# Performance work log

Measured on AMD Instinct MI355X. Metric: run time of the kernel, lower is better.

The kernel has to match this reference:

```python
import math
import jax, jax.numpy as jnp
import numpy as np

VMIN, VMAX, NUM_BINS = 0.0, 1.0, 64
BIN_WIDTH = (VMAX - VMIN) / NUM_BINS
SIGMA = BIN_WIDTH * (1.0 / (2.0 * math.sqrt(2.0 * math.log(2.0))))
EPS = 1e-10


def setup_inputs() -> dict:
    key = jax.random.key(0)
    kx, ky = jax.random.split(key)
    shape = (2, 1, 96, 96, 96)
    x = jax.random.uniform(kx, shape, dtype=jnp.float32)
    y = jax.random.uniform(ky, shape, dtype=jnp.float32)
    return {"x": x, "y": y}


def _gauss_win(v, bins):
    # v: (N, P), bins: (B,) -> (N, B, P)
    d = v[:, None, :] - bins[None, :, None]
    # NOTE: faithful to source: exp(.)/sqrt(2*pi) * sigma (multiplies by sigma)
    return jnp.exp(-(d * d) / (2.0 * SIGMA * SIGMA)) / math.sqrt(2.0 * math.pi) * SIGMA


def reference(x, y):
    N = x.shape[0]
    xf = x.reshape(N, -1)  # (N, P); dim=1 channel folded into P
    yf = y.reshape(N, -1)
    bins = jnp.linspace(VMIN, VMAX, NUM_BINS, dtype=x.dtype)
    win_x = _gauss_win(xf, bins)  # (N, B, P)
    win_y = _gauss_win(yf, bins)  # (N, B, P)
    hist_joint = jnp.einsum('nbp,ncp->nbc', win_x, win_y)  # (N, B, B)
    hist_norm = hist_joint.sum(axis=(1, 2)) + EPS
    p_joint = hist_joint / hist_norm[:, None, None]
    p_x = p_joint.sum(axis=2)
    p_y = p_joint.sum(axis=1)
    ent_x = -jnp.sum(p_x * jnp.log(p_x + EPS), axis=1)
    ent_y = -jnp.sum(p_y * jnp.log(p_y + EPS), axis=1)
    ent_joint = -jnp.sum(p_joint * jnp.log(p_joint + EPS), axis=(1, 2))
    # normalised=True branch
    return -jnp.mean((ent_x + ent_y) / ent_joint)
```

## Files before the change

kernel.cpp:

```cpp
#include <hip/hip_runtime.h>
#include <math.h>


#define NBINS 64
#define BK 240
#define LDA 248
#define NKB 15

typedef _Float16 half8    __attribute__((ext_vector_type(8)));
typedef float    floatx16 __attribute__((ext_vector_type(16)));

static constexpr double kSigmaD = 0.015625 / 2.3548200450309493;
static constexpr double kAcD    = (1.0 / (63.0 * 63.0)) / (2.0 * kSigmaD * kSigmaD);
static constexpr float  kAc     = (float)kAcD;
static constexpr float  kEps    = 1e-10f;

__device__ __forceinline__ void make_weights(float vx, float vy, bool valid,
                                             int& cx, int& cy,
                                             float* wx, float* wy) {
    cx = 2; cy = 2;
#pragma unroll
    for (int k = 0; k < 5; ++k) { wx[k] = 0.0f; wy[k] = 0.0f; }
    if (valid) {
        cx = min(max((int)(vx + 0.5f), 2), 61);
        cy = min(max((int)(vy + 0.5f), 2), 61);
        const float dx = vx - (float)cx;
        const float dy = vy - (float)cy;
#pragma unroll
        for (int k = 0; k < 5; ++k) {
            const float ddx = dx - (float)(k - 2);
            const float ddy = dy - (float)(k - 2);
            wx[k] = __expf(-kAc * ddx * ddx);
            wy[k] = __expf(-kAc * ddy * ddy);
        }
    }
}

__global__ __launch_bounds__(256) void hist_gemm_kernel(
        const float* __restrict__ x, const float* __restrict__ y,
        float* __restrict__ hist, int P, int elemsPerBlock) {
    __shared__ __align__(16) _Float16 tiles[2 * NBINS * LDA];
    _Float16* Ax = tiles;
    _Float16* By = tiles + NBINS * LDA;

    const int t    = threadIdx.x;
    const int lane = t & 63;
    const int wave = t >> 6;
    const int m    = lane & 31;
    const int kq   = 8 * (lane >> 5);
    const int n    = blockIdx.y;

    {
        float* z4 = (float*)tiles;
        const int ndw = 2 * NBINS * LDA / 2;
        for (int i = t; i < ndw; i += 256) z4[i] = 0.0f;
    }

    floatx16 acc[2][2];
#pragma unroll
    for (int bi = 0; bi < 2; ++bi)
#pragma unroll
        for (int bj = 0; bj < 2; ++bj) acc[bi][bj] = (floatx16){};

    const float* __restrict__ xp = x + (size_t)n * P;
    const float* __restrict__ yp = y + (size_t)n * P;
    const int base    = blockIdx.x * elemsPerBlock;
    const int nElems  = elemsPerBlock;
    const int nChunks = (nElems + BK - 1) / BK;

    int cx, cy; float wx[5], wy[5];
    {
        const bool valid = (t < BK) && (t < nElems);
        float vx = 0.0f, vy = 0.0f;
        if (valid) { vx = xp[base + t] * 63.0f; vy = yp[base + t] * 63.0f; }
        make_weights(vx, vy, valid, cx, cy, wx, wy);
    }
    int pcx = 2, pcy = 2;
    __syncthreads();

    for (int c = 0; c < nChunks; ++c) {
        if (t < BK) {
#pragma unroll
            for (int k = 0; k < 5; ++k) {
                Ax[(pcx - 2 + k) * LDA + t] = (_Float16)0.0f;
                By[(pcy - 2 + k) * LDA + t] = (_Float16)0.0f;
            }
#pragma unroll
            for (int k = 0; k < 5; ++k) {
                Ax[(cx - 2 + k) * LDA + t] = (_Float16)wx[k];
                By[(cy - 2 + k) * LDA + t] = (_Float16)wy[k];
            }
        }
        pcx = cx; pcy = cy;
        __syncthreads();

        float vx = 0.0f, vy = 0.0f; bool valid = false;
        if (c + 1 < nChunks) {
            const int off = (c + 1) * BK + t;
            valid = (t < BK) && (off < nElems);
            if (valid) { vx = xp[base + off] * 63.0f; vy = yp[base + off] * 63.0f; }
        }

#pragma unroll
        for (int s = 0; s < 4; ++s) {
            const int kb = wave + 4 * s;
            if (kb >= NKB) break;
            const int ko = kb * 16 + kq;
            const half8 a0 = *(const half8*)&Ax[m * LDA + ko];
            const half8 a1 = *(const half8*)&Ax[(32 + m) * LDA + ko];
            const half8 b0 = *(const half8*)&By[m * LDA + ko];
            const half8 b1 = *(const half8*)&By[(32 + m) * LDA + ko];
            acc[0][0] = __builtin_amdgcn_mfma_f32_32x32x16_f16(a0, b0, acc[0][0], 0, 0, 0);
            acc[0][1] = __builtin_amdgcn_mfma_f32_32x32x16_f16(a0, b1, acc[0][1], 0, 0, 0);
            acc[1][0] = __builtin_amdgcn_mfma_f32_32x32x16_f16(a1, b0, acc[1][0], 0, 0, 0);
            acc[1][1] = __builtin_amdgcn_mfma_f32_32x32x16_f16(a1, b1, acc[1][1], 0, 0, 0);
        }

        make_weights(vx, vy, valid, cx, cy, wx, wy);
        __syncthreads();
    }

    float* cred = (float*)tiles;
    const int rbase = 4 * (lane >> 5);

    if (wave >= 2) {
        const int off = (wave - 2) * 4096;
#pragma unroll
        for (int bi = 0; bi < 2; ++bi)
#pragma unroll
            for (int bj = 0; bj < 2; ++bj)
#pragma unroll
                for (int r = 0; r < 16; ++r) {
                    const int row = bi * 32 + (r & 3) + 8 * (r >> 2) + rbase;
                    const int col = bj * 32 + m;
                    cred[off + row * NBINS + col] = acc[bi][bj][r];
                }
    }
    __syncthreads();
    if (wave < 2) {
        const int off = wave * 4096;
#pragma unroll
        for (int bi = 0; bi < 2; ++bi)
#pragma unroll
            for (int bj = 0; bj < 2; ++bj)
#pragma unroll
                for (int r = 0; r < 16; ++r) {
                    const int row = bi * 32 + (r & 3) + 8 * (r >> 2) + rbase;
                    const int col = bj * 32 + m;
                    const int idx = off + row * NBINS + col;
                    cred[idx] = acc[bi][bj][r] + cred[idx];
                }
    }
    __syncthreads();
    float* __restrict__ gh = hist + (size_t)n * NBINS * NBINS;
    for (int i = t; i < NBINS * NBINS; i += 256)
        atomicAdd(&gh[i], cred[i] + cred[4096 + i]);
}

__device__ __forceinline__ float block_sum_bcast(float v, float* sm) {
#pragma unroll
    for (int off = 32; off > 0; off >>= 1) v += __shfl_down(v, off, 64);
    __syncthreads();
    const int lane = threadIdx.x & 63;
    const int wid  = threadIdx.x >> 6;
    if (lane == 0) sm[wid] = v;
    __syncthreads();
    return sm[0] + sm[1] + sm[2] + sm[3];
}

__global__ __launch_bounds__(256) void finalize_kernel(
        const float* __restrict__ hist, float* __restrict__ out) {
    __shared__ float sm[4];
    __shared__ float sx[NBINS];
    __shared__ float sy[NBINS];

    const int n = blockIdx.x;
    const float* __restrict__ h = hist + (size_t)n * NBINS * NBINS;

    float s = 0.0f;
    for (int i = threadIdx.x; i < NBINS * NBINS; i += 256) s += h[i];
    const float S = block_sum_bcast(s, sm) + kEps;
    const float invS = 1.0f / S;

    float ej = 0.0f;
    for (int i = threadIdx.x; i < NBINS * NBINS; i += 256) {
        const float p = h[i] * invS;
        ej += p * __logf(p + kEps);
    }

    if (threadIdx.x < NBINS) {
        float px = 0.0f;
        const float* rp = &h[threadIdx.x * NBINS];
        for (int c = 0; c < NBINS; c++) px += rp[c];
        px *= invS;
        sx[threadIdx.x] = px * __logf(px + kEps);
    } else if (threadIdx.x < 2 * NBINS) {
        const int c = threadIdx.x - NBINS;
        float py = 0.0f;
        for (int b = 0; b < NBINS; b++) py += h[b * NBINS + c];
        py *= invS;
        sy[c] = py * __logf(py + kEps);
    }

    const float EJ = block_sum_bcast(ej, sm);
    const float mx = (threadIdx.x < NBINS) ? sx[threadIdx.x] : 0.0f;
    const float my = (threadIdx.x < NBINS) ? sy[threadIdx.x] : 0.0f;
    const float EX = block_sum_bcast(mx, sm);
    const float EY = block_sum_bcast(my, sm);

    if (threadIdx.x == 0) atomicAdd(out, -0.5f * ((EX + EY) / EJ));
}

extern "C" void kernel_launch(void* const* d_in, const int* in_sizes, int n_in,
                              void* d_out, int out_size, void* d_ws, size_t ws_size,
                              hipStream_t stream) {
    const float* x = (const float*)d_in[0];
    const float* y = (const float*)d_in[1];
    float* hist = (float*)d_ws;
    float* out  = (float*)d_out;

    const int N = 2;
    const int P = in_sizes[0] / N;
    const int blocksPerN = 256;
    const int elemsPerBlock = P / blocksPerN;

    hipMemsetAsync(hist, 0, (size_t)N * NBINS * NBINS * sizeof(float), stream);
    hipMemsetAsync(out, 0, sizeof(float), stream);

    dim3 grid(blocksPerN, N);
    hist_gemm_kernel<<<grid, 256, 0, stream>>>(x, y, hist, P, elemsPerBlock);

    finalize_kernel<<<2, 256, 0, stream>>>(hist, out);
}
```

Measured before the change: 107.8 us.

## Split output quadrants across waves, shrink K chunk, and raise block count

Each wave now owns one 32x32 quadrant of the 64x64 joint histogram and runs the full K range of each chunk, replacing the earlier scheme where waves split K and summed four accumulators. The chunk size drops to 112 elements, blocksPerN grows to 576, and launch bounds request more resident blocks. The intermediate shared-memory reduction goes away and each wave atomically adds its accumulators straight to global memory. The aim is more parallelism and less per-block reduction work, at the cost of more global atomics and more blocks contending on the same histogram entries.

```diff
diff --git a/kernel.cpp b/kernel.cpp
--- a/kernel.cpp
+++ b/kernel.cpp
@@ -3,9 +3,9 @@
 
 
 #define NBINS 64
-#define BK 240
-#define LDA 248
-#define NKB 15
+#define BK 112
+#define LDA 120
+#define NKB 7
 
 typedef _Float16 half8    __attribute__((ext_vector_type(8)));
 typedef float    floatx16 __attribute__((ext_vector_type(16)));
@@ -36,7 +36,7 @@
     }
 }
 
-__global__ __launch_bounds__(256) void hist_gemm_kernel(
+__global__ __launch_bounds__(256, 4) void hist_gemm_kernel(
         const float* __restrict__ x, const float* __restrict__ y,
         float* __restrict__ hist, int P, int elemsPerBlock) {
     __shared__ __align__(16) _Float16 tiles[2 * NBINS * LDA];
@@ -48,6 +48,8 @@
     const int wave = t >> 6;
     const int m    = lane & 31;
     const int kq   = 8 * (lane >> 5);
+    const int qi   = wave >> 1;
+    const int qj   = wave & 1;
     const int n    = blockIdx.y;
 
     {
@@ -56,11 +58,7 @@
         for (int i = t; i < ndw; i += 256) z4[i] = 0.0f;
     }
 
-    floatx16 acc[2][2];
-#pragma unroll
-    for (int bi = 0; bi < 2; ++bi)
-#pragma unroll
-        for (int bj = 0; bj < 2; ++bj) acc[bi][bj] = (floatx16){};
+    floatx16 acc = {};
 
     const float* __restrict__ xp = x + (size_t)n * P;
     const float* __restrict__ yp = y + (size_t)n * P;
@@ -101,60 +99,27 @@
             if (valid) { vx = xp[base + off] * 63.0f; vy = yp[base + off] * 63.0f; }
         }
 
+        const int rA = qi * 32 + m;
+        const int rB = qj * 32 + m;
 #pragma unroll
-        for (int s = 0; s < 4; ++s) {
-            const int kb = wave + 4 * s;
-            if (kb >= NKB) break;
-            const int ko = kb * 16 + kq;
-            const half8 a0 = *(const half8*)&Ax[m * LDA + ko];
-            const half8 a1 = *(const half8*)&Ax[(32 + m) * LDA + ko];
-            const half8 b0 = *(const half8*)&By[m * LDA + ko];
-            const half8 b1 = *(const half8*)&By[(32 + m) * LDA + ko];
-            acc[0][0] = __builtin_amdgcn_mfma_f32_32x32x16_f16(a0, b0, acc[0][0], 0, 0, 0);
-            acc[0][1] = __builtin_amdgcn_mfma_f32_32x32x16_f16(a0, b1, acc[0][1], 0, 0, 0);
-            acc[1][0] = __builtin_amdgcn_mfma_f32_32x32x16_f16(a1, b0, acc[1][0], 0, 0, 0);
-            acc[1][1] = __builtin_amdgcn_mfma_f32_32x32x16_f16(a1, b1, acc[1][1], 0, 0, 0);
+        for (int kb = 0; kb < NKB; ++kb) {
+            const half8 a = *(const half8*)&Ax[rA * LDA + kb * 16 + kq];
+            const half8 b = *(const half8*)&By[rB * LDA + kb * 16 + kq];
+            acc = __builtin_amdgcn_mfma_f32_32x32x16_f16(a, b, acc, 0, 0, 0);
         }
 
         make_weights(vx, vy, valid, cx, cy, wx, wy);
         __syncthreads();
     }
 
-    float* cred = (float*)tiles;
+    float* __restrict__ gh = hist + (size_t)n * NBINS * NBINS;
     const int rbase = 4 * (lane >> 5);
-
-    if (wave >= 2) {
-        const int off = (wave - 2) * 4096;
 #pragma unroll
-        for (int bi = 0; bi < 2; ++bi)
-#pragma unroll
-            for (int bj = 0; bj < 2; ++bj)
-#pragma unroll
-                for (int r = 0; r < 16; ++r) {
-                    const int row = bi * 32 + (r & 3) + 8 * (r >> 2) + rbase;
-                    const int col = bj * 32 + m;
-                    cred[off + row * NBINS + col] = acc[bi][bj][r];
-                }
+    for (int r = 0; r < 16; ++r) {
+        const int row = qi * 32 + (r & 3) + 8 * (r >> 2) + rbase;
+        const int col = qj * 32 + m;
+        atomicAdd(&gh[row * NBINS + col], acc[r]);
     }
-    __syncthreads();
-    if (wave < 2) {
-        const int off = wave * 4096;
-#pragma unroll
-        for (int bi = 0; bi < 2; ++bi)
-#pragma unroll
-            for (int bj = 0; bj < 2; ++bj)
-#pragma unroll
-                for (int r = 0; r < 16; ++r) {
-                    const int row = bi * 32 + (r & 3) + 8 * (r >> 2) + rbase;
-                    const int col = bj * 32 + m;
-                    const int idx = off + row * NBINS + col;
-                    cred[idx] = acc[bi][bj][r] + cred[idx];
-                }
-    }
-    __syncthreads();
-    float* __restrict__ gh = hist + (size_t)n * NBINS * NBINS;
-    for (int i = t; i < NBINS * NBINS; i += 256)
-        atomicAdd(&gh[i], cred[i] + cred[4096 + i]);
 }
 
 __device__ __forceinline__ float block_sum_bcast(float v, float* sm) {
@@ -221,7 +186,7 @@
 
     const int N = 2;
     const int P = in_sizes[0] / N;
-    const int blocksPerN = 256;
+    const int blocksPerN = 576;
     const int elemsPerBlock = P / blocksPerN;
 
     hipMemsetAsync(hist, 0, (size_t)N * NBINS * NBINS * sizeof(float), stream);
```

After: 109.5 us. No clear change (+1.5%).

## Double-buffer swizzled LDS tiles and split x/y weight generation across threads

Applied to the files above, without the earlier changes.

Switches from a single padded tile with chunk size 240 to double-buffered 64x128 fp16 tiles with an XOR swizzle in place of padding to avoid LDS bank conflicts. Half the threads now build the x weights and half the y weights, so all 256 threads do useful work, and the next chunk's tile is written while MFMAs read the current one. This removes one barrier per chunk. It also requests two blocks per CU through launch bounds. The cost is twice the LDS footprint, and it relies on elemsPerBlock being divisible by 128 (it is 3456 = 27*128).

```diff
diff --git a/kernel.cpp b/kernel.cpp
--- a/kernel.cpp
+++ b/kernel.cpp
@@ -3,9 +3,12 @@
 
 
 #define NBINS 64
-#define BK 240
-#define LDA 248
-#define NKB 15
+#define BK 128
+#define TILE (NBINS * BK)
+#define NKB 8
+
+#define SWZ(r) ((((r) >> 3) ^ (r)) & 7)
+#define CHIDX(r, c) ((r) * BK + ((((c) & 8) | (((c) ^ SWZ(r)) & 7)) << 3))
 
 typedef _Float16 half8    __attribute__((ext_vector_type(8)));
 typedef float    floatx16 __attribute__((ext_vector_type(16)));
@@ -15,45 +18,33 @@
 static constexpr float  kAc     = (float)kAcD;
 static constexpr float  kEps    = 1e-10f;
 
-__device__ __forceinline__ void make_weights(float vx, float vy, bool valid,
-                                             int& cx, int& cy,
-                                             float* wx, float* wy) {
-    cx = 2; cy = 2;
-#pragma unroll
-    for (int k = 0; k < 5; ++k) { wx[k] = 0.0f; wy[k] = 0.0f; }
-    if (valid) {
-        cx = min(max((int)(vx + 0.5f), 2), 61);
-        cy = min(max((int)(vy + 0.5f), 2), 61);
-        const float dx = vx - (float)cx;
-        const float dy = vy - (float)cy;
-#pragma unroll
-        for (int k = 0; k < 5; ++k) {
-            const float ddx = dx - (float)(k - 2);
-            const float ddy = dy - (float)(k - 2);
-            wx[k] = __expf(-kAc * ddx * ddx);
-            wy[k] = __expf(-kAc * ddy * ddy);
-        }
-    }
-}
-
-__global__ __launch_bounds__(256) void hist_gemm_kernel(
+__device__ __forceinline__ void make_w(float v, int& c, float* w) {
+    c = min(max((int)(v + 0.5f), 2), 61);
+    const float d = v - (float)c;
+#pragma unroll
+    for (int k = 0; k < 5; ++k) {
+        const float dd = d - (float)(k - 2);
+        w[k] = __expf(-kAc * dd * dd);
+    }
+}
+
+__global__ __launch_bounds__(256, 2) void hist_gemm_kernel(
         const float* __restrict__ x, const float* __restrict__ y,
         float* __restrict__ hist, int P, int elemsPerBlock) {
-    __shared__ __align__(16) _Float16 tiles[2 * NBINS * LDA];
-    _Float16* Ax = tiles;
-    _Float16* By = tiles + NBINS * LDA;
+    __shared__ __align__(16) _Float16 tiles[4 * TILE];
 
     const int t    = threadIdx.x;
     const int lane = t & 63;
     const int wave = t >> 6;
     const int m    = lane & 31;
-    const int kq   = 8 * (lane >> 5);
+    const int kq8  = lane >> 5;
     const int n    = blockIdx.y;
+    const int col  = t & 127;
+    const bool isX = (t < 128);
 
     {
         float* z4 = (float*)tiles;
-        const int ndw = 2 * NBINS * LDA / 2;
-        for (int i = t; i < ndw; i += 256) z4[i] = 0.0f;
+        for (int i = t; i < 4 * TILE / 2; i += 256) z4[i] = 0.0f;
     }
 
     floatx16 acc[2][2];
@@ -62,66 +53,75 @@
 #pragma unroll
         for (int bj = 0; bj < 2; ++bj) acc[bi][bj] = (floatx16){};
 
-    const float* __restrict__ xp = x + (size_t)n * P;
-    const float* __restrict__ yp = y + (size_t)n * P;
+    const float* __restrict__ src = (isX ? x : y) + (size_t)n * P;
     const int base    = blockIdx.x * elemsPerBlock;
-    const int nElems  = elemsPerBlock;
-    const int nChunks = (nElems + BK - 1) / BK;
-
-    int cx, cy; float wx[5], wy[5];
+    const int nChunks = elemsPerBlock / BK;
+
+    _Float16* myTile = tiles + (isX ? 0 : TILE);
+    const int cc0 = col >> 3;
+    const int cw  = col & 7;
+
+    int pc[2] = {2, 2};
+
     {
-        const bool valid = (t < BK) && (t < nElems);
-        float vx = 0.0f, vy = 0.0f;
-        if (valid) { vx = xp[base + t] * 63.0f; vy = yp[base + t] * 63.0f; }
-        make_weights(vx, vy, valid, cx, cy, wx, wy);
-    }
-    int pcx = 2, pcy = 2;
+        int ctr; float w[5];
+        make_w(src[base + col] * 63.0f, ctr, w);
+#pragma unroll
+        for (int k = 0; k < 5; ++k) {
+            const int r = ctr - 2 + k;
+            myTile[CHIDX(r, cc0) + cw] = (_Float16)w[k];
+        }
+        pc[0] = ctr;
+    }
     __syncthreads();
 
     for (int c = 0; c < nChunks; ++c) {
-        if (t < BK) {
-#pragma unroll
-            for (int k = 0; k < 5; ++k) {
-                Ax[(pcx - 2 + k) * LDA + t] = (_Float16)0.0f;
-                By[(pcy - 2 + k) * LDA + t] = (_Float16)0.0f;
-            }
-#pragma unroll
-            for (int k = 0; k < 5; ++k) {
-                Ax[(cx - 2 + k) * LDA + t] = (_Float16)wx[k];
-                By[(cy - 2 + k) * LDA + t] = (_Float16)wy[k];
-            }
-        }
-        pcx = cx; pcy = cy;
-        __syncthreads();
-
-        float vx = 0.0f, vy = 0.0f; bool valid = false;
-        if (c + 1 < nChunks) {
-            const int off = (c + 1) * BK + t;
-            valid = (t < BK) && (off < nElems);
-            if (valid) { vx = xp[base + off] * 63.0f; vy = yp[base + off] * 63.0f; }
-        }
-
-#pragma unroll
-        for (int s = 0; s < 4; ++s) {
+        const int b  = c & 1;
+        const int nb = b ^ 1;
+        const bool more = (c + 1 < nChunks);
+
+        float v = 0.0f;
+        if (more) v = src[base + (c + 1) * BK + col] * 63.0f;
+
+        const _Float16* Axb = tiles + b * 2 * TILE;
+        const _Float16* Byb = Axb + TILE;
+#pragma unroll
+        for (int s = 0; s < 2; ++s) {
             const int kb = wave + 4 * s;
-            if (kb >= NKB) break;
-            const int ko = kb * 16 + kq;
-            const half8 a0 = *(const half8*)&Ax[m * LDA + ko];
-            const half8 a1 = *(const half8*)&Ax[(32 + m) * LDA + ko];
-            const half8 b0 = *(const half8*)&By[m * LDA + ko];
-            const half8 b1 = *(const half8*)&By[(32 + m) * LDA + ko];
+            const int ch = 2 * kb + kq8;
+            const int r0 = m, r1 = 32 + m;
+            const half8 a0 = *(const half8*)&Axb[CHIDX(r0, ch)];
+            const half8 a1 = *(const half8*)&Axb[CHIDX(r1, ch)];
+            const half8 b0 = *(const half8*)&Byb[CHIDX(r0, ch)];
+            const half8 b1 = *(const half8*)&Byb[CHIDX(r1, ch)];
             acc[0][0] = __builtin_amdgcn_mfma_f32_32x32x16_f16(a0, b0, acc[0][0], 0, 0, 0);
             acc[0][1] = __builtin_amdgcn_mfma_f32_32x32x16_f16(a0, b1, acc[0][1], 0, 0, 0);
             acc[1][0] = __builtin_amdgcn_mfma_f32_32x32x16_f16(a1, b0, acc[1][0], 0, 0, 0);
             acc[1][1] = __builtin_amdgcn_mfma_f32_32x32x16_f16(a1, b1, acc[1][1], 0, 0, 0);
         }
 
-        make_weights(vx, vy, valid, cx, cy, wx, wy);
+        if (more) {
+            int ctr; float w[5];
+            make_w(v, ctr, w);
+            _Float16* st = myTile + nb * 2 * TILE;
+            const int po = pc[nb];
+#pragma unroll
+            for (int k = 0; k < 5; ++k) {
+                const int r = po - 2 + k;
+                st[CHIDX(r, cc0) + cw] = (_Float16)0.0f;
+            }
+#pragma unroll
+            for (int k = 0; k < 5; ++k) {
+                const int r = ctr - 2 + k;
+                st[CHIDX(r, cc0) + cw] = (_Float16)w[k];
+            }
+            pc[nb] = ctr;
+        }
         __syncthreads();
     }
 
     float* cred = (float*)tiles;
-    const int rbase = 4 * (lane >> 5);
+    const int rbase = 4 * kq8;
 
     if (wave >= 2) {
         const int off = (wave - 2) * 4096;
@@ -132,8 +132,8 @@
 #pragma unroll
                 for (int r = 0; r < 16; ++r) {
                     const int row = bi * 32 + (r & 3) + 8 * (r >> 2) + rbase;
-                    const int col = bj * 32 + m;
-                    cred[off + row * NBINS + col] = acc[bi][bj][r];
+                    const int cl  = bj * 32 + m;
+                    cred[off + row * NBINS + cl] = acc[bi][bj][r];
                 }
     }
     __syncthreads();
@@ -146,8 +146,8 @@
 #pragma unroll
                 for (int r = 0; r < 16; ++r) {
                     const int row = bi * 32 + (r & 3) + 8 * (r >> 2) + rbase;
-                    const int col = bj * 32 + m;
-                    const int idx = off + row * NBINS + col;
+                    const int cl  = bj * 32 + m;
+                    const int idx = off + row * NBINS + cl;
                     cred[idx] = acc[bi][bj][r] + cred[idx];
                 }
     }
```

New measurement: 108.1 us. About the same (+0.2%).
